# Kernel tuning notes

Measured on AMD Instinct MI355X. Metric: run time of the kernel, lower is better.

## Reference

```python
import jax, jax.numpy as jnp
import numpy as np

B, S, IN_DIM, D_MODEL, H = 1, 4096, 512, 512, 8
DK = D_MODEL // H


def setup_inputs() -> dict:
    key = jax.random.key(0)
    ks = jax.random.split(key, 10)
    sc_in = 1.0 / np.sqrt(IN_DIM)
    sc_dm = 1.0 / np.sqrt(D_MODEL)
    return {
        "x": jax.random.normal(ks[0], (B, S, IN_DIM), dtype=jnp.float32),
        "mask": jax.random.randint(ks[1], (1, 1, S, S), 0, 2, dtype=jnp.int32),
        "wq_w": jax.random.uniform(ks[2], (D_MODEL, IN_DIM), jnp.float32, -sc_in, sc_in),
        "wq_b": jax.random.uniform(ks[3], (D_MODEL,), jnp.float32, -sc_in, sc_in),
        "wk_w": jax.random.uniform(ks[4], (D_MODEL, IN_DIM), jnp.float32, -sc_in, sc_in),
        "wk_b": jax.random.uniform(ks[5], (D_MODEL,), jnp.float32, -sc_in, sc_in),
        "wv_w": jax.random.uniform(ks[6], (D_MODEL, IN_DIM), jnp.float32, -sc_in, sc_in),
        "wv_b": jax.random.uniform(ks[7], (D_MODEL,), jnp.float32, -sc_in, sc_in),
        "dense_w": jax.random.uniform(ks[8], (D_MODEL, D_MODEL), jnp.float32, -sc_dm, sc_dm),
        "dense_b": jax.random.uniform(ks[9], (D_MODEL,), jnp.float32, -sc_dm, sc_dm),
    }


def _split_heads(t):
    # Faithful to original: raw view [B, S, D] -> [B, H, S, DK] (no transpose)
    return t.reshape(B, H, S, DK)


def reference(x, mask, wq_w, wq_b, wk_w, wk_b, wv_w, wv_b, dense_w, dense_b):
    q = _split_heads(x @ wq_w.T + wq_b)  # [B, H, S, DK]
    k = _split_heads(x @ wk_w.T + wk_b)
    v = _split_heads(x @ wv_w.T + wv_b)
    score = jnp.einsum("bhqd,bhkd->bhqk", q, k) / np.sqrt(DK).astype(np.float32)
    score = score + mask.astype(score.dtype) * (-1e9)
    attn = jax.nn.softmax(score, axis=-1)
    out = jnp.einsum("bhqk,bhkd->bhqd", attn, v)  # [B, H, S, DK]
    out = out.transpose(0, 2, 1, 3).reshape(B, S, D_MODEL)
    return out @ dense_w.T + dense_b
```

## Files before the change

### kernel.cpp

```cpp
#include <hip/hip_runtime.h>
#include <hip/hip_bf16.h>

#define S_LEN 4096
#define DM    512
#define NH    8
#define DK    64

typedef __attribute__((ext_vector_type(8))) __bf16 bf16x8;
typedef __attribute__((ext_vector_type(4))) float  f32x4;
typedef unsigned short u16;
typedef unsigned int   u32;
typedef unsigned long long u64;

#define SQ_SCALE (0.125f * 1.44269504f)
#define FMAX 12.0f

#define NPART 4
#define KSPAN 1024

__device__ __forceinline__ u16 f2bf(float f) {
  union { float f; u32 i; } v; v.f = f;
  u32 r = v.i + 0x7fff + ((v.i >> 16) & 1);
  return (u16)(r >> 16);
}
__device__ __forceinline__ float bf2f(u16 u) {
  union { u32 i; float f; } v; v.i = ((u32)u) << 16; return v.f;
}

__device__ __forceinline__ void gl_lds16(const u16* g, u16* l) {
  __builtin_amdgcn_global_load_lds(
      (const __attribute__((address_space(1))) u32*)g,
      (__attribute__((address_space(3))) u32*)l, 16, 0, 0);
}

__global__ __launch_bounds__(256) void pack_mask(const int* __restrict__ mask,
                                                 u64* __restrict__ out) {
  int gid = blockIdx.x * 256 + threadIdx.x;
  u64 b = __ballot(mask[gid] != 0);
  if ((threadIdx.x & 63) == 0) out[gid >> 6] = b;
}

__global__ __launch_bounds__(256) void convert_all(
    const float* __restrict__ x, const float* __restrict__ wq,
    const float* __restrict__ wk, const float* __restrict__ wv,
    const float* __restrict__ dw,
    u16* __restrict__ xb, u16* __restrict__ wcat, u16* __restrict__ dwb) {
  int b = blockIdx.x;
  const float* src; u16* dst; size_t off;
  if      (b < 2048) { src = x;  dst = xb;   off = (size_t)b * 1024; }
  else if (b < 2304) { src = wq; dst = wcat; off = (size_t)(b - 2048) * 1024; }
  else if (b < 2560) { src = wk; dst = wcat + 262144; off = (size_t)(b - 2304) * 1024; }
  else if (b < 2816) { src = wv; dst = wcat + 524288; off = (size_t)(b - 2560) * 1024; }
  else               { src = dw; dst = dwb;  off = (size_t)(b - 2816) * 1024; }
  size_t i = off + (size_t)threadIdx.x * 4;
  float4 v = *reinterpret_cast<const float4*>(src + i);
  ushort4 o = make_ushort4(f2bf(v.x), f2bf(v.y), f2bf(v.z), f2bf(v.w));
  *reinterpret_cast<ushort4*>(dst + i) = o;
}

__global__ __launch_bounds__(256) void qkv_gemm(
    const u16* __restrict__ A, const u16* __restrict__ Wcat,
    const float* __restrict__ bq, const float* __restrict__ bk,
    const float* __restrict__ bv,
    u16* __restrict__ Qb, u16* __restrict__ Kb, u16* __restrict__ V4) {
  __shared__ u16 As[64 * 72];
  __shared__ u16 Ws[128 * 72];
  const int t = threadIdx.x;
  const int lane = t & 63, wv = t >> 6;
  const int m16 = lane & 15, quad = lane >> 4;
  const int n0g = blockIdx.x * 128, m0 = blockIdx.y * 64;
  const int seg = n0g >> 9;
  const int n0 = n0g & 511;
  const int mq = wv >> 1, nq = wv & 1;

  f32x4 acc[2][4];
#pragma unroll
  for (int i = 0; i < 2; i++)
#pragma unroll
    for (int j = 0; j < 4; j++) acc[i][j] = (f32x4)0.f;

  for (int k0 = 0; k0 < DM; k0 += 64) {
    __syncthreads();
#pragma unroll
    for (int c0 = 0; c0 < 2; c0++) {
      int c = t + c0 * 256;
      int row = c >> 3, col = (c & 7) * 8;
      *reinterpret_cast<uint4*>(&As[row * 72 + col]) =
          *reinterpret_cast<const uint4*>(&A[(size_t)(m0 + row) * DM + k0 + col]);
    }
#pragma unroll
    for (int c0 = 0; c0 < 4; c0++) {
      int c = t + c0 * 256;
      int row = c >> 3, col = (c & 7) * 8;
      *reinterpret_cast<uint4*>(&Ws[row * 72 + col]) =
          *reinterpret_cast<const uint4*>(&Wcat[(size_t)(n0g + row) * DM + k0 + col]);
    }
    __syncthreads();
#pragma unroll
    for (int kk = 0; kk < 64; kk += 32) {
      bf16x8 a0 = *reinterpret_cast<const bf16x8*>(&As[(mq * 32 + m16) * 72 + quad * 8 + kk]);
      bf16x8 a1 = *reinterpret_cast<const bf16x8*>(&As[(mq * 32 + 16 + m16) * 72 + quad * 8 + kk]);
#pragma unroll
      for (int ct = 0; ct < 4; ct++) {
        bf16x8 b = *reinterpret_cast<const bf16x8*>(&Ws[(nq * 64 + ct * 16 + m16) * 72 + quad * 8 + kk]);
        acc[0][ct] = __builtin_amdgcn_mfma_f32_16x16x32_bf16(a0, b, acc[0][ct], 0, 0, 0);
        acc[1][ct] = __builtin_amdgcn_mfma_f32_16x16x32_bf16(a1, b, acc[1][ct], 0, 0, 0);
      }
    }
  }

  const float* bias = (seg == 0) ? bq : (seg == 1) ? bk : bv;
  const float scale = (seg == 0) ? SQ_SCALE : 1.f;
  float bn[4];
#pragma unroll
  for (int ct = 0; ct < 4; ct++) bn[ct] = bias[n0 + nq * 64 + ct * 16 + m16];

  if (seg == 2) {
    __syncthreads();
    u16* T = Ws;
#pragma unroll
    for (int rt = 0; rt < 2; rt++)
#pragma unroll
      for (int ct = 0; ct < 4; ct++)
#pragma unroll
        for (int r = 0; r < 4; r++)
          T[(nq * 64 + ct * 16 + m16) * 72 + mq * 32 + rt * 16 + quad * 4 + r] =
              f2bf(acc[rt][ct][r] + bn[ct]);
    __syncthreads();
    const int h    = m0 >> 9;
    const int mp   = m0 & 511;
    const int cseg = n0 >> 7;
#pragma unroll
    for (int c0 = 0; c0 < 4; c0++) {
      int c = t + c0 * 256;
      int d  = c >> 4;
      int tl = (c >> 1) & 7;
      int cl = c & 1;
      uint4 v = *reinterpret_cast<const uint4*>(&T[(cl * 64 + d) * 72 + tl * 8]);
      *reinterpret_cast<uint4*>(
          &V4[(size_t)(h * 64 + d) * 4096 + ((mp >> 3) + tl) * 64 + cl * 32 + cseg * 8]) = v;
    }
  } else {
    u16* dst = (seg == 0) ? Qb : Kb;
#pragma unroll
    for (int rt = 0; rt < 2; rt++)
#pragma unroll
      for (int ct = 0; ct < 4; ct++) {
        int n = n0 + nq * 64 + ct * 16 + m16;
#pragma unroll
        for (int r = 0; r < 4; r++) {
          int m = m0 + mq * 32 + rt * 16 + quad * 4 + r;
          dst[(size_t)m * DM + n] = f2bf((acc[rt][ct][r] + bn[ct]) * scale);
        }
      }
  }
}

__global__ __launch_bounds__(256) void dense_gemm(
    const u16* __restrict__ A, const u16* __restrict__ W,
    const float* __restrict__ bias, float* __restrict__ Cout) {
  __shared__ u16 As[64 * 72];
  __shared__ u16 Ws[64 * 72];
  const int t = threadIdx.x;
  const int lane = t & 63, wv = t >> 6;
  const int m16 = lane & 15, quad = lane >> 4;
  const int n0 = blockIdx.x * 64, m0 = blockIdx.y * 64;

  f32x4 acc[4];
#pragma unroll
  for (int j = 0; j < 4; j++) acc[j] = (f32x4)0.f;

  for (int k0 = 0; k0 < DM; k0 += 64) {
    __syncthreads();
#pragma unroll
    for (int c0 = 0; c0 < 2; c0++) {
      int c = t + c0 * 256;
      int row = c >> 3, col = (c & 7) * 8;
      *reinterpret_cast<uint4*>(&As[row * 72 + col]) =
          *reinterpret_cast<const uint4*>(&A[(size_t)(m0 + row) * DM + k0 + col]);
      *reinterpret_cast<uint4*>(&Ws[row * 72 + col]) =
          *reinterpret_cast<const uint4*>(&W[(size_t)(n0 + row) * DM + k0 + col]);
    }
    __syncthreads();
#pragma unroll
    for (int kk = 0; kk < 64; kk += 32) {
      bf16x8 a = *reinterpret_cast<const bf16x8*>(&As[(wv * 16 + m16) * 72 + quad * 8 + kk]);
#pragma unroll
      for (int ct = 0; ct < 4; ct++) {
        bf16x8 b = *reinterpret_cast<const bf16x8*>(&Ws[(ct * 16 + m16) * 72 + quad * 8 + kk]);
        acc[ct] = __builtin_amdgcn_mfma_f32_16x16x32_bf16(a, b, acc[ct], 0, 0, 0);
      }
    }
  }

  float bn[4];
#pragma unroll
  for (int ct = 0; ct < 4; ct++) bn[ct] = bias[n0 + ct * 16 + m16];
#pragma unroll
  for (int ct = 0; ct < 4; ct++) {
    int n = n0 + ct * 16 + m16;
#pragma unroll
    for (int r = 0; r < 4; r++) {
      int m = m0 + wv * 16 + quad * 4 + r;
      Cout[(size_t)m * DM + n] = acc[ct][r] + bn[ct];
    }
  }
}

__device__ __forceinline__ void pack_p(const f32x4* s, u32 lo, u32 hi,
                                       uint4& o0, uint4& o1) {
  u32 pk[8];
#pragma unroll
  for (int ct = 0; ct < 4; ct++) {
    u32 w = (ct & 1) ? hi : lo;
    int b = ct >> 1;
    float p0 = __builtin_amdgcn_exp2f(((w >> b) & 1u)        ? -1e9f : s[ct][0]);
    float p1 = __builtin_amdgcn_exp2f(((w >> (b + 8)) & 1u)  ? -1e9f : s[ct][1]);
    float p2 = __builtin_amdgcn_exp2f(((w >> (b + 16)) & 1u) ? -1e9f : s[ct][2]);
    float p3 = __builtin_amdgcn_exp2f(((w >> (b + 24)) & 1u) ? -1e9f : s[ct][3]);
    pk[2 * ct]     = __builtin_amdgcn_perm(__float_as_uint(p1) + 0x8000u,
                                           __float_as_uint(p0) + 0x8000u, 0x07060302u);
    pk[2 * ct + 1] = __builtin_amdgcn_perm(__float_as_uint(p3) + 0x8000u,
                                           __float_as_uint(p2) + 0x8000u, 0x07060302u);
  }
  o0 = make_uint4(pk[0], pk[1], pk[2], pk[3]);
  o1 = make_uint4(pk[4], pk[5], pk[6], pk[7]);
}

__global__ __launch_bounds__(256, 4) void attn_mfma(
    const u16* __restrict__ Q, const u16* __restrict__ K,
    const u16* __restrict__ V4, const u64* __restrict__ mbits,
    u16* __restrict__ Op, float* __restrict__ Lp) {
  __shared__ u16 Ks[2][64 * 64];
  __shared__ u16 Vs[2][64 * 64];

  const int t = threadIdx.x;
  const int lane = t & 63, w4 = t >> 6;
  const int m16 = lane & 15, quad = lane >> 4;
  const int lin = blockIdx.x;
  const int q0 = ((lin >> 3) & 31) * 128;
  const int hg = ((lin >> 8) << 3) | (lin & 7);
  const int h = hg & 7;
  const int g = hg >> 3;
  const size_t hoff = (size_t)h * S_LEN * DK;
  const size_t kbase = hoff + (size_t)g * KSPAN * DK;

  const u16* qpA = Q + hoff + (size_t)(q0 + w4 * 32 + m16) * DK + quad * 8;
  bf16x8 qloA = *reinterpret_cast<const bf16x8*>(qpA);
  bf16x8 qhiA = *reinterpret_cast<const bf16x8*>(qpA + 32);
  bf16x8 qloB = *reinterpret_cast<const bf16x8*>(qpA + 16 * DK);
  bf16x8 qhiB = *reinterpret_cast<const bf16x8*>(qpA + 16 * DK + 32);

  union { u16 u[8]; bf16x8 v; } onesu;
#pragma unroll
  for (int j = 0; j < 8; j++) onesu.u[j] = 0x3F80;
  const bf16x8 ones = onesu.v;

  const int l = lane;
  const int colu = ((l & 7) ^ (l >> 3)) * 8;
  const u16* kp[2]; const u16* vp[2]; int ldso[2];
#pragma unroll
  for (int i = 0; i < 2; i++) {
    int row = (w4 * 2 + i) * 8 + (l >> 3);
    int inv = (((row >> 4) & 1) << 5) | (((row >> 1) & 1) << 4) | ((row & 1) << 3) |
              (((row >> 3) & 1) << 2) | (((row >> 2) & 1) << 1) | ((row >> 5) & 1);
    kp[i] = K + kbase + (size_t)inv * DK + colu;
    vp[i] = V4 + (size_t)(h * 64 + row) * 4096 + g * KSPAN + colu;
    ldso[i] = (w4 * 2 + i) * 512 + l * 8;
  }

  const u64* mpA = &mbits[(size_t)(q0 + w4 * 32 + m16) * 64 + ((g * KSPAN) >> 6)];
  const u64* mpB = mpA + (size_t)16 * 64;

  f32x4 accA[4], accB[4];
  f32x4 acc_lA = (f32x4)0.f, acc_lB = (f32x4)0.f;
#pragma unroll
  for (int dt = 0; dt < 4; dt++) { accA[dt] = (f32x4)0.f; accB[dt] = (f32x4)0.f; }

#pragma unroll
  for (int i = 0; i < 2; i++) {
    gl_lds16(kp[i], &Ks[0][ldso[i]]);
    gl_lds16(vp[i], &Vs[0][ldso[i]]);
  }
  u64 rmA = mpA[0], rmB = mpB[0];
  __syncthreads();

  const int xorv = (m16 & 7) * 8;
  int cur = 0;
#pragma unroll 1
  for (int k0 = 0; k0 < KSPAN; k0 += 64) {
    if (k0 + 64 < KSPAN) {
#pragma unroll
      for (int i = 0; i < 2; i++) {
        gl_lds16(kp[i] + (size_t)(k0 + 64) * DK, &Ks[cur ^ 1][ldso[i]]);
        gl_lds16(vp[i] + (k0 + 64),              &Vs[cur ^ 1][ldso[i]]);
      }
    }
    u64 mqA = rmA >> (2 * quad);
    u64 mqB = rmB >> (2 * quad);
    if (k0 + 64 < KSPAN) { rmA = mpA[(k0 >> 6) + 1]; rmB = mpB[(k0 >> 6) + 1]; }

    const u16* Kc = Ks[cur];
    const u16* Vc = Vs[cur];

    f32x4 sA[4], sB[4];
#pragma unroll
    for (int ct = 0; ct < 4; ct++) { sA[ct] = (f32x4)(-FMAX); sB[ct] = (f32x4)(-FMAX); }
#pragma unroll
    for (int ct = 0; ct < 4; ct++) {
      const int rb = (ct * 16 + m16) * 64;
      bf16x8 klo = *reinterpret_cast<const bf16x8*>(&Kc[rb + ((quad * 8) ^ xorv)]);
      bf16x8 khi = *reinterpret_cast<const bf16x8*>(&Kc[rb + ((quad * 8 + 32) ^ xorv)]);
      sA[ct] = __builtin_amdgcn_mfma_f32_16x16x32_bf16(klo, qloA, sA[ct], 0, 0, 0);
      sA[ct] = __builtin_amdgcn_mfma_f32_16x16x32_bf16(khi, qhiA, sA[ct], 0, 0, 0);
      sB[ct] = __builtin_amdgcn_mfma_f32_16x16x32_bf16(klo, qloB, sB[ct], 0, 0, 0);
      sB[ct] = __builtin_amdgcn_mfma_f32_16x16x32_bf16(khi, qhiB, sB[ct], 0, 0, 0);
    }

    union { uint4 i; bf16x8 v; } pA0, pA1, pB0, pB1;
    pack_p(sA, (u32)mqA, (u32)(mqA >> 32), pA0.i, pA1.i);
    pack_p(sB, (u32)mqB, (u32)(mqB >> 32), pB0.i, pB1.i);

#pragma unroll
    for (int dt = 0; dt < 4; dt++) {
      const int rb = (dt * 16 + m16) * 64;
      bf16x8 vlo = *reinterpret_cast<const bf16x8*>(&Vc[rb + ((quad * 8) ^ xorv)]);
      bf16x8 vhi = *reinterpret_cast<const bf16x8*>(&Vc[rb + ((quad * 8 + 32) ^ xorv)]);
      accA[dt] = __builtin_amdgcn_mfma_f32_16x16x32_bf16(pA0.v, vlo, accA[dt], 0, 0, 0);
      accA[dt] = __builtin_amdgcn_mfma_f32_16x16x32_bf16(pA1.v, vhi, accA[dt], 0, 0, 0);
      accB[dt] = __builtin_amdgcn_mfma_f32_16x16x32_bf16(pB0.v, vlo, accB[dt], 0, 0, 0);
      accB[dt] = __builtin_amdgcn_mfma_f32_16x16x32_bf16(pB1.v, vhi, accB[dt], 0, 0, 0);
    }
    acc_lA = __builtin_amdgcn_mfma_f32_16x16x32_bf16(pA0.v, ones, acc_lA, 0, 0, 0);
    acc_lA = __builtin_amdgcn_mfma_f32_16x16x32_bf16(pA1.v, ones, acc_lA, 0, 0, 0);
    acc_lB = __builtin_amdgcn_mfma_f32_16x16x32_bf16(pB0.v, ones, acc_lB, 0, 0, 0);
    acc_lB = __builtin_amdgcn_mfma_f32_16x16x32_bf16(pB1.v, ones, acc_lB, 0, 0, 0);

    __syncthreads();
    cur ^= 1;
  }

  u16* Og = Op + (size_t)g * 2097152;
#pragma unroll
  for (int dt = 0; dt < 4; dt++)
#pragma unroll
    for (int r = 0; r < 4; r++) {
      Og[(size_t)(q0 + w4 * 32 + quad * 4 + r) * DM + h * DK + dt * 16 + m16] =
          f2bf(accA[dt][r]);
      Og[(size_t)(q0 + w4 * 32 + 16 + quad * 4 + r) * DM + h * DK + dt * 16 + m16] =
          f2bf(accB[dt][r]);
    }
  if (m16 == 0) {
#pragma unroll
    for (int r = 0; r < 4; r++) {
      Lp[g * 32768 + h * 4096 + q0 + w4 * 32 + quad * 4 + r] = acc_lA[r];
      Lp[g * 32768 + h * 4096 + q0 + w4 * 32 + 16 + quad * 4 + r] = acc_lB[r];
    }
  }
}

__global__ __launch_bounds__(256) void attn_merge(
    const u16* __restrict__ Op, const float* __restrict__ Lp,
    u16* __restrict__ Out) {
  int i8 = (blockIdx.x * 256 + threadIdx.x) * 8;
  int q = i8 >> 9;
  int h = (i8 >> 6) & 7;
  float l = 0.f;
#pragma unroll
  for (int part = 0; part < NPART; part++) l += Lp[part * 32768 + h * 4096 + q];
  float rl = 1.f / l;
  float o[8];
#pragma unroll
  for (int j = 0; j < 8; j++) o[j] = 0.f;
#pragma unroll
  for (int part = 0; part < NPART; part++) {
    ushort4 v0 = *reinterpret_cast<const ushort4*>(Op + (size_t)part * 2097152 + i8);
    ushort4 v1 = *reinterpret_cast<const ushort4*>(Op + (size_t)part * 2097152 + i8 + 4);
    o[0] += bf2f(v0.x); o[1] += bf2f(v0.y); o[2] += bf2f(v0.z); o[3] += bf2f(v0.w);
    o[4] += bf2f(v1.x); o[5] += bf2f(v1.y); o[6] += bf2f(v1.z); o[7] += bf2f(v1.w);
  }
  ushort4 o0 = make_ushort4(f2bf(o[0] * rl), f2bf(o[1] * rl),
                            f2bf(o[2] * rl), f2bf(o[3] * rl));
  ushort4 o1 = make_ushort4(f2bf(o[4] * rl), f2bf(o[5] * rl),
                            f2bf(o[6] * rl), f2bf(o[7] * rl));
  *reinterpret_cast<ushort4*>(Out + i8) = o0;
  *reinterpret_cast<ushort4*>(Out + i8 + 4) = o1;
}

extern "C" void kernel_launch(void* const* d_in, const int* in_sizes, int n_in,
                              void* d_out, int out_size, void* d_ws, size_t ws_size,
                              hipStream_t stream) {
  const float* x    = (const float*)d_in[0];
  const int*   mask = (const int*)d_in[1];
  const float* wq_w = (const float*)d_in[2];
  const float* wq_b = (const float*)d_in[3];
  const float* wk_w = (const float*)d_in[4];
  const float* wk_b = (const float*)d_in[5];
  const float* wv_w = (const float*)d_in[6];
  const float* wv_b = (const float*)d_in[7];
  const float* dw   = (const float*)d_in[8];
  const float* db   = (const float*)d_in[9];

  u16* xb    = (u16*)d_ws;
  u16* wcat  = xb    + 2097152;
  u16* dwb   = wcat  + 786432;
  u16* Qb    = dwb   + 262144;
  u16* Kb    = Qb    + 2097152;
  u16* V4    = Kb    + 2097152;
  u16* Opart = V4    + 2097152;
  u64* mb    = (u64*)(Opart + (size_t)NPART * 2097152);
  float* Lp  = (float*)(mb + 262144);

  pack_mask<<<(S_LEN * S_LEN) / 256, 256, 0, stream>>>(mask, mb);
  convert_all<<<3072, 256, 0, stream>>>(x, wq_w, wk_w, wv_w, dw, xb, wcat, dwb);

  qkv_gemm<<<dim3(12, 64), 256, 0, stream>>>(xb, wcat, wq_b, wk_b, wv_b,
                                             Qb, Kb, V4);

  attn_mfma<<<1024, 256, 0, stream>>>(Qb, Kb, V4, mb, Opart, Lp);
  attn_merge<<<1024, 256, 0, stream>>>(Opart, Lp, Qb);

  dense_gemm<<<dim3(8, 64), 256, 0, stream>>>(Qb, dwb, db, (float*)d_out);
}
```

Before: 218.6 us.

## Double-buffer GEMM tiles with direct global-to-LDS loads and XOR swizzle

Both projection GEMMs (QKV and dense) now use two LDS buffers, filled through direct global-to-LDS loads (gl_lds16). The next K tile is prefetched while MFMAs run on the current one, which removes one barrier per iteration and overlaps memory latency with compute. Padded rows are replaced by an XOR column swizzle to avoid LDS bank conflicts without wasting space. This doubles LDS use and relies on the closing barrier of the loop to keep buffer reuse correct. The attention kernel, likely the bulk of the runtime, is untouched.

Measured after the change: 219.7 us. Within noise of the previous version (+0.5%).

```diff
diff --git a/kernel.cpp b/kernel.cpp
--- a/kernel.cpp
+++ b/kernel.cpp
@@ -63,8 +63,8 @@
     const float* __restrict__ bq, const float* __restrict__ bk,
     const float* __restrict__ bv,
     u16* __restrict__ Qb, u16* __restrict__ Kb, u16* __restrict__ V4) {
-  __shared__ u16 As[64 * 72];
-  __shared__ u16 Ws[128 * 72];
+  __shared__ u16 As[2][64 * 64];
+  __shared__ u16 Ws[2][128 * 64];
   const int t = threadIdx.x;
   const int lane = t & 63, wv = t >> 6;
   const int m16 = lane & 15, quad = lane >> 4;
@@ -73,40 +73,62 @@
   const int n0 = n0g & 511;
   const int mq = wv >> 1, nq = wv & 1;
 
+  const u16* asrc[2]; int ldsoA[2];
+#pragma unroll
+  for (int c0 = 0; c0 < 2; c0++) {
+    int c = t + c0 * 256;
+    int row = c >> 3, swc = ((c & 7) ^ (row & 7)) * 8;
+    asrc[c0] = A + (size_t)(m0 + row) * DM + swc;
+    ldsoA[c0] = c * 8;
+  }
+  const u16* wsrc[4]; int ldsoW[4];
+#pragma unroll
+  for (int c0 = 0; c0 < 4; c0++) {
+    int c = t + c0 * 256;
+    int row = c >> 3, swc = ((c & 7) ^ (row & 7)) * 8;
+    wsrc[c0] = Wcat + (size_t)(n0g + row) * DM + swc;
+    ldsoW[c0] = c * 8;
+  }
+
   f32x4 acc[2][4];
 #pragma unroll
   for (int i = 0; i < 2; i++)
 #pragma unroll
     for (int j = 0; j < 4; j++) acc[i][j] = (f32x4)0.f;
 
+#pragma unroll
+  for (int c0 = 0; c0 < 2; c0++) gl_lds16(asrc[c0], &As[0][ldsoA[c0]]);
+#pragma unroll
+  for (int c0 = 0; c0 < 4; c0++) gl_lds16(wsrc[c0], &Ws[0][ldsoW[c0]]);
+  __syncthreads();
+
+  const int xorv = m16 & 7;
+  int cur = 0;
   for (int k0 = 0; k0 < DM; k0 += 64) {
-    __syncthreads();
-#pragma unroll
-    for (int c0 = 0; c0 < 2; c0++) {
-      int c = t + c0 * 256;
-      int row = c >> 3, col = (c & 7) * 8;
-      *reinterpret_cast<uint4*>(&As[row * 72 + col]) =
-          *reinterpret_cast<const uint4*>(&A[(size_t)(m0 + row) * DM + k0 + col]);
-    }
-#pragma unroll
-    for (int c0 = 0; c0 < 4; c0++) {
-      int c = t + c0 * 256;
-      int row = c >> 3, col = (c & 7) * 8;
-      *reinterpret_cast<uint4*>(&Ws[row * 72 + col]) =
-          *reinterpret_cast<const uint4*>(&Wcat[(size_t)(n0g + row) * DM + k0 + col]);
-    }
-    __syncthreads();
+    if (k0 + 64 < DM) {
+#pragma unroll
+      for (int c0 = 0; c0 < 2; c0++)
+        gl_lds16(asrc[c0] + k0 + 64, &As[cur ^ 1][ldsoA[c0]]);
+#pragma unroll
+      for (int c0 = 0; c0 < 4; c0++)
+        gl_lds16(wsrc[c0] + k0 + 64, &Ws[cur ^ 1][ldsoW[c0]]);
+    }
+    const u16* Ac = As[cur];
+    const u16* Wc = Ws[cur];
 #pragma unroll
     for (int kk = 0; kk < 64; kk += 32) {
-      bf16x8 a0 = *reinterpret_cast<const bf16x8*>(&As[(mq * 32 + m16) * 72 + quad * 8 + kk]);
-      bf16x8 a1 = *reinterpret_cast<const bf16x8*>(&As[(mq * 32 + 16 + m16) * 72 + quad * 8 + kk]);
+      const int gcol = (((quad + (kk >> 3)) ^ xorv) * 8);
+      bf16x8 a0 = *reinterpret_cast<const bf16x8*>(&Ac[(mq * 32 + m16) * 64 + gcol]);
+      bf16x8 a1 = *reinterpret_cast<const bf16x8*>(&Ac[(mq * 32 + 16 + m16) * 64 + gcol]);
 #pragma unroll
       for (int ct = 0; ct < 4; ct++) {
-        bf16x8 b = *reinterpret_cast<const bf16x8*>(&Ws[(nq * 64 + ct * 16 + m16) * 72 + quad * 8 + kk]);
+        bf16x8 b = *reinterpret_cast<const bf16x8*>(&Wc[(nq * 64 + ct * 16 + m16) * 64 + gcol]);
         acc[0][ct] = __builtin_amdgcn_mfma_f32_16x16x32_bf16(a0, b, acc[0][ct], 0, 0, 0);
         acc[1][ct] = __builtin_amdgcn_mfma_f32_16x16x32_bf16(a1, b, acc[1][ct], 0, 0, 0);
       }
     }
+    __syncthreads();
+    cur ^= 1;
   }
 
   const float* bias = (seg == 0) ? bq : (seg == 1) ? bk : bv;
@@ -116,8 +138,7 @@
   for (int ct = 0; ct < 4; ct++) bn[ct] = bias[n0 + nq * 64 + ct * 16 + m16];
 
   if (seg == 2) {
-    __syncthreads();
-    u16* T = Ws;
+    u16* T = &Ws[0][0];
 #pragma unroll
     for (int rt = 0; rt < 2; rt++)
 #pragma unroll
@@ -159,38 +180,58 @@
 __global__ __launch_bounds__(256) void dense_gemm(
     const u16* __restrict__ A, const u16* __restrict__ W,
     const float* __restrict__ bias, float* __restrict__ Cout) {
-  __shared__ u16 As[64 * 72];
-  __shared__ u16 Ws[64 * 72];
+  __shared__ u16 As[2][64 * 64];
+  __shared__ u16 Ws[2][64 * 64];
   const int t = threadIdx.x;
   const int lane = t & 63, wv = t >> 6;
   const int m16 = lane & 15, quad = lane >> 4;
   const int n0 = blockIdx.x * 64, m0 = blockIdx.y * 64;
 
+  const u16* asrc[2]; const u16* wsrc[2]; int ldso[2];
+#pragma unroll
+  for (int c0 = 0; c0 < 2; c0++) {
+    int c = t + c0 * 256;
+    int row = c >> 3, swc = ((c & 7) ^ (row & 7)) * 8;
+    asrc[c0] = A + (size_t)(m0 + row) * DM + swc;
+    wsrc[c0] = W + (size_t)(n0 + row) * DM + swc;
+    ldso[c0] = c * 8;
+  }
+
   f32x4 acc[4];
 #pragma unroll
   for (int j = 0; j < 4; j++) acc[j] = (f32x4)0.f;
 
+#pragma unroll
+  for (int c0 = 0; c0 < 2; c0++) {
+    gl_lds16(asrc[c0], &As[0][ldso[c0]]);
+    gl_lds16(wsrc[c0], &Ws[0][ldso[c0]]);
+  }
+  __syncthreads();
+
+  const int xorv = m16 & 7;
+  int cur = 0;
   for (int k0 = 0; k0 < DM; k0 += 64) {
-    __syncthreads();
-#pragma unroll
-    for (int c0 = 0; c0 < 2; c0++) {
-      int c = t + c0 * 256;
-      int row = c >> 3, col = (c & 7) * 8;
-      *reinterpret_cast<uint4*>(&As[row * 72 + col]) =
-          *reinterpret_cast<const uint4*>(&A[(size_t)(m0 + row) * DM + k0 + col]);
-      *reinterpret_cast<uint4*>(&Ws[row * 72 + col]) =
-          *reinterpret_cast<const uint4*>(&W[(size_t)(n0 + row) * DM + k0 + col]);
-    }
-    __syncthreads();
+    if (k0 + 64 < DM) {
+#pragma unroll
+      for (int c0 = 0; c0 < 2; c0++) {
+        gl_lds16(asrc[c0] + k0 + 64, &As[cur ^ 1][ldso[c0]]);
+        gl_lds16(wsrc[c0] + k0 + 64, &Ws[cur ^ 1][ldso[c0]]);
+      }
+    }
+    const u16* Ac = As[cur];
+    const u16* Wc = Ws[cur];
 #pragma unroll
     for (int kk = 0; kk < 64; kk += 32) {
-      bf16x8 a = *reinterpret_cast<const bf16x8*>(&As[(wv * 16 + m16) * 72 + quad * 8 + kk]);
+      const int gcol = (((quad + (kk >> 3)) ^ xorv) * 8);
+      bf16x8 a = *reinterpret_cast<const bf16x8*>(&Ac[(wv * 16 + m16) * 64 + gcol]);
 #pragma unroll
       for (int ct = 0; ct < 4; ct++) {
-        bf16x8 b = *reinterpret_cast<const bf16x8*>(&Ws[(ct * 16 + m16) * 72 + quad * 8 + kk]);
+        bf16x8 b = *reinterpret_cast<const bf16x8*>(&Wc[(ct * 16 + m16) * 64 + gcol]);
         acc[ct] = __builtin_amdgcn_mfma_f32_16x16x32_bf16(a, b, acc[ct], 0, 0, 0);
       }
     }
+    __syncthreads();
+    cur ^= 1;
   }
 
   float bn[4];
```
